# Kernel optimization log

Hardware: AMD Instinct MI355X
Metric: run time of the kernel (lower is better)

The kernel has to match this reference:

```python
import jax, jax.numpy as jnp
import numpy as np


def setup_inputs() -> dict:
    key = jax.random.key(0)
    kq, kk, kv, kl = jax.random.split(key, 4)
    B, Nq, Nkv, D = 16, 2048, 2048, 64
    return {
        "Q_batch": jax.random.normal(kq, (B, Nq, D), dtype=jnp.float32),
        "K_batch": jax.random.normal(kk, (B, Nkv, D), dtype=jnp.float32),
        "V_batch": jax.random.normal(kv, (B, Nkv, D), dtype=jnp.float32),
        "valid_lens": jax.random.randint(kl, (B,), 0, Nkv, dtype=jnp.int64 if jax.config.jax_enable_x64 else jnp.int32),
    }


def reference(Q_batch, K_batch, V_batch, valid_lens):
    # S: (B, Nq, Nkv) scaled dot-product scores
    d = Q_batch.shape[-1]
    scale = 1.0 / jnp.sqrt(jnp.asarray(d, Q_batch.dtype))
    S = jnp.einsum('bqd,bkd->bqk', Q_batch, K_batch) * scale
    # mask_first_n_valid: position k valid iff k < valid_lens[b], broadcast over queries
    kv_idx = jnp.arange(S.shape[-1])  # (Nkv,)
    mask = kv_idx[None, None, :] < valid_lens[:, None, None]  # (B, 1->Nq, Nkv)
    S = jnp.where(mask, S, jnp.asarray(-1e20, S.dtype))
    W = jax.nn.softmax(S, axis=-1)  # attention weights (dropout rate = 0.0)
    return jnp.einsum('bqk,bkv->bqv', W, V_batch)
```

## Files before the change

### kernel.cpp

```cpp
#include <hip/hip_runtime.h>

#define BATCH 16
#define NQ    2048
#define NKV   2048
#define DH    64
#define SC    0.18033688011112042f
#define TILE_B 8192

typedef __attribute__((ext_vector_type(8))) short  bf16x8;
typedef __attribute__((ext_vector_type(16))) float f32x16;

__device__ __forceinline__ unsigned f2bf(float f) {
  unsigned u = __builtin_bit_cast(unsigned, f);
  u += 0x7FFFu + ((u >> 16) & 1u);
  return u >> 16;
}

template <int CTRL>
__device__ __forceinline__ float dppf(float x) {
  return __builtin_bit_cast(
      float, __builtin_amdgcn_mov_dpp(__builtin_bit_cast(int, x), CTRL, 0xF, 0xF, false));
}
__device__ __forceinline__ float rowsum16(float v) {
  v += dppf<0x128>(v);
  v += dppf<0x124>(v);
  v += dppf<0x122>(v);
  v += dppf<0x121>(v);
  return v;
}

__global__ __launch_bounds__(256) void convert_kernel(
    const float* __restrict__ K, const float* __restrict__ V,
    unsigned char* __restrict__ WS) {
  const int tid = threadIdx.x;
  const int bt  = blockIdx.x;
  const int b   = bt >> 6, t = bt & 63;
  unsigned char* tile = WS + (size_t)bt * TILE_B;
  const size_t   srow = ((size_t)b * NKV + (size_t)t * 32) * DH;

  const int l = tid & 63, g = tid >> 6;
  {
    const int key = l & 31, d0 = g * 16 + (l >> 5) * 8;
    const float4* p = (const float4*)(K + srow + (size_t)key * DH + d0);
    float4 a = p[0], c4 = p[1];
    bf16x8 w;
    w[0] = (short)f2bf(a.x);  w[1] = (short)f2bf(a.y);
    w[2] = (short)f2bf(a.z);  w[3] = (short)f2bf(a.w);
    w[4] = (short)f2bf(c4.x); w[5] = (short)f2bf(c4.y);
    w[6] = (short)f2bf(c4.z); w[7] = (short)f2bf(c4.w);
    *(bf16x8*)(tile + g * 1024 + l * 16) = w;
  }
  {
    const int d    = (g & 1) * 32 + (l & 31);
    const int key0 = (g >> 1) * 16 + (l >> 5) * 8;
    const float* vp = V + srow + (size_t)key0 * DH + d;
    bf16x8 w;
#pragma unroll
    for (int j = 0; j < 8; ++j) w[j] = (short)f2bf(vp[(size_t)j * DH]);
    *(bf16x8*)(tile + 4096 + g * 1024 + l * 16) = w;
  }
}

__global__ __launch_bounds__(256, 4) void sdpa_kernel(
    const float* __restrict__ Q, const unsigned char* __restrict__ WS,
    const int* __restrict__ lens, float* __restrict__ O) {
  __shared__ alignas(16) unsigned char smem[10240 + 2 * 12288];

  const int tid  = threadIdx.x;
  const int lane = tid & 63;
  const int wave = tid >> 6;
  const int k32  = lane & 31;
  const int hi   = lane >> 5;

  const int idx = blockIdx.x, layer = idx >> 8, rr = idx & 255;
  const int b   = (rr + layer * 3) & 15;
  const int qo  = (rr >> 4) + layer * 16;

  const int  L    = lens[b];
  const bool zlen = (L == 0);
  const int  Leff = zlen ? NKV : L;
  const int  nT   = (Leff + 31) >> 5;
  const int  tb   = (nT * wave) >> 2;
  const int  te   = (nT * (wave + 1)) >> 2;
  const int  cnt  = te - tb;
  const int  tmask = (!zlen && (L & 31)) ? nT - 1 : -1;

  bf16x8 Qf[4];
  {
    const float* qp = Q + ((size_t)b * NQ + qo * 32 + k32) * DH + hi * 8;
#pragma unroll
    for (int c = 0; c < 4; ++c) {
      const float4* p = (const float4*)(qp + c * 16);
      float4 a = p[0], d4 = p[1];
      bf16x8 w;
      w[0] = (short)f2bf(a.x * SC);  w[1] = (short)f2bf(a.y * SC);
      w[2] = (short)f2bf(a.z * SC);  w[3] = (short)f2bf(a.w * SC);
      w[4] = (short)f2bf(d4.x * SC); w[5] = (short)f2bf(d4.y * SC);
      w[6] = (short)f2bf(d4.z * SC); w[7] = (short)f2bf(d4.w * SC);
      Qf[c] = w;
    }
  }

  unsigned char*       Pw  = smem + wave * 2560;
  unsigned char*       pwr = Pw + hi * 320 + k32 * 2;
  const unsigned char* prd = Pw + k32 * 80 + hi * 16;

  const unsigned char* gp = WS + (size_t)(b * 64 + tb) * TILE_B + lane * 16;

  f32x16 oc0, oc1;
  float  l_[16];
#pragma unroll
  for (int r = 0; r < 16; ++r) { oc0[r] = 0.f; oc1[r] = 0.f; l_[r] = 0.f; }

  for (int it = 0; it < cnt; ++it) {
    bf16x8 cur[8];
#pragma unroll
    for (int i = 0; i < 8; ++i) cur[i] = *(const bf16x8*)(gp + i * 1024);
    gp += TILE_B;

    const int t = tb + it;

    f32x16 acc;
#pragma unroll
    for (int r = 0; r < 16; ++r) acc[r] = 0.f;
#pragma unroll
    for (int c = 0; c < 4; ++c)
      acc = __builtin_amdgcn_mfma_f32_32x32x16_bf16(Qf[c], cur[c], acc, 0, 0, 0);

    if (zlen) {
#pragma unroll
      for (int r = 0; r < 16; ++r) acc[r] = 0.f;
    } else if (t == tmask) {
      const bool valid = (t * 32 + k32) < L;
      if (!valid) {
#pragma unroll
        for (int r = 0; r < 16; ++r) acc[r] = -1e30f;
      }
    }

#pragma unroll
    for (int r = 0; r < 16; ++r) {
      float    p = __builtin_amdgcn_exp2f(acc[r]);
      unsigned u = __builtin_bit_cast(unsigned, p);
      l_[r] += __builtin_bit_cast(float, u & 0xFFFF0000u);
      *(unsigned short*)(pwr + ((r & 3) + 8 * (r >> 2)) * 80) =
          (unsigned short)(u >> 16);
    }

#pragma unroll
    for (int ks = 0; ks < 2; ++ks) {
      bf16x8 Pf = *(const bf16x8*)(prd + ks * 32);
      oc0 = __builtin_amdgcn_mfma_f32_32x32x16_bf16(Pf, cur[4 + ks * 2], oc0, 0, 0, 0);
      oc1 = __builtin_amdgcn_mfma_f32_32x32x16_bf16(Pf, cur[5 + ks * 2], oc1, 0, 0, 0);
    }
  }

  float* MS = (float*)(void*)(smem + 10240);
  __syncthreads();
  if (wave >= 2) {
    float* Mb = MS + (wave - 2) * 3072 + lane;
#pragma unroll
    for (int r = 0; r < 16; ++r) {
      Mb[r * 64] = l_[r]; Mb[(16 + r) * 64] = oc0[r]; Mb[(32 + r) * 64] = oc1[r];
    }
  }
  __syncthreads();
  if (wave < 2) {
    float* Mb = MS + wave * 3072 + lane;
#pragma unroll
    for (int r = 0; r < 16; ++r) {
      l_[r] += Mb[r * 64]; oc0[r] += Mb[(16 + r) * 64]; oc1[r] += Mb[(32 + r) * 64];
    }
  }
  __syncthreads();
  if (wave == 1) {
    float* Mb = MS + lane;
#pragma unroll
    for (int r = 0; r < 16; ++r) {
      Mb[r * 64] = l_[r]; Mb[(16 + r) * 64] = oc0[r]; Mb[(32 + r) * 64] = oc1[r];
    }
  }
  __syncthreads();
  if (wave == 0) {
    float* Mb = MS + lane;
#pragma unroll
    for (int r = 0; r < 16; ++r) {
      l_[r] += Mb[r * 64]; oc0[r] += Mb[(16 + r) * 64]; oc1[r] += Mb[(32 + r) * 64];
    }
    float* Ob = O + ((size_t)b * NQ + qo * 32) * DH;
#pragma unroll
    for (int r = 0; r < 16; ++r) {
      float s = rowsum16(l_[r]);
      s += __builtin_bit_cast(
          float, __builtin_amdgcn_ds_swizzle(__builtin_bit_cast(int, s), 0x401F));
      const float inv = 1.0f / s;
      const int   q   = (r & 3) + 8 * (r >> 2) + 4 * hi;
      Ob[q * DH + k32]      = oc0[r] * inv;
      Ob[q * DH + 32 + k32] = oc1[r] * inv;
    }
  }
}

extern "C" void kernel_launch(void* const* d_in, const int* in_sizes, int n_in,
                              void* d_out, int out_size, void* d_ws, size_t ws_size,
                              hipStream_t stream) {
  const float* Q    = (const float*)d_in[0];
  const float* K    = (const float*)d_in[1];
  const float* V    = (const float*)d_in[2];
  const int*   lens = (const int*)d_in[3];
  float*       Out  = (float*)d_out;
  unsigned char* WS = (unsigned char*)d_ws;

  hipLaunchKernelGGL(convert_kernel, dim3(BATCH * 64), dim3(256), 0, stream, K, V, WS);
  hipLaunchKernelGGL(sdpa_kernel, dim3(1024), dim3(256), 0, stream, Q, WS, lens, Out);
}
```

Before: 97.86 us.

## Process 64 queries per block, keep P in registers, prefetch next KV tile

Each block now handles 64 queries (two 32-row Q fragments), so every loaded K/V tile is reused twice and the grid is halved. The MFMA operands are swapped so the P tile comes out in a layout that can feed the PV MFMA straight from registers, which drops the LDS round trip for P. The V tile layout in the convert kernel is changed to match. The next tile is loaded into registers while the current one is computed, and the output is staged through LDS for coalesced float4 stores. The convert kernel also skips tiles past the valid length. Costs are higher register pressure (launch bounds lowered to 2) and fewer blocks, which may leave some CUs idle.

```diff
diff --git a/kernel.cpp b/kernel.cpp
--- a/kernel.cpp
+++ b/kernel.cpp
@@ -16,32 +16,22 @@
   return u >> 16;
 }
 
-template <int CTRL>
-__device__ __forceinline__ float dppf(float x) {
-  return __builtin_bit_cast(
-      float, __builtin_amdgcn_mov_dpp(__builtin_bit_cast(int, x), CTRL, 0xF, 0xF, false));
-}
-__device__ __forceinline__ float rowsum16(float v) {
-  v += dppf<0x128>(v);
-  v += dppf<0x124>(v);
-  v += dppf<0x122>(v);
-  v += dppf<0x121>(v);
-  return v;
-}
-
 __global__ __launch_bounds__(256) void convert_kernel(
     const float* __restrict__ K, const float* __restrict__ V,
-    unsigned char* __restrict__ WS) {
-  const int tid = threadIdx.x;
-  const int bt  = blockIdx.x;
-  const int b   = bt >> 6, t = bt & 63;
+    const int* __restrict__ lens, unsigned char* __restrict__ WS) {
+  const int bt = blockIdx.x;
+  const int b = bt >> 6, t = bt & 63;
+  const int L = lens[b];
+  const int Leff = (L == 0) ? NKV : L;
+  if (t * 32 >= Leff) return;
+
   unsigned char* tile = WS + (size_t)bt * TILE_B;
   const size_t   srow = ((size_t)b * NKV + (size_t)t * 32) * DH;
-
+  const int tid = threadIdx.x;
   const int l = tid & 63, g = tid >> 6;
+  const int l31 = l & 31, hi = l >> 5;
   {
-    const int key = l & 31, d0 = g * 16 + (l >> 5) * 8;
-    const float4* p = (const float4*)(K + srow + (size_t)key * DH + d0);
+    const float4* p = (const float4*)(K + srow + (size_t)l31 * DH + g * 16 + hi * 8);
     float4 a = p[0], c4 = p[1];
     bf16x8 w;
     w[0] = (short)f2bf(a.x);  w[1] = (short)f2bf(a.y);
@@ -51,26 +41,25 @@
     *(bf16x8*)(tile + g * 1024 + l * 16) = w;
   }
   {
-    const int d    = (g & 1) * 32 + (l & 31);
-    const int key0 = (g >> 1) * 16 + (l >> 5) * 8;
-    const float* vp = V + srow + (size_t)key0 * DH + d;
+    const int c2 = g & 1, dh = g >> 1;
+    const float* vp = V + srow + (size_t)(c2 * 16 + 4 * hi) * DH + dh * 32 + l31;
     bf16x8 w;
 #pragma unroll
-    for (int j = 0; j < 8; ++j) w[j] = (short)f2bf(vp[(size_t)j * DH]);
+    for (int j = 0; j < 8; ++j)
+      w[j] = (short)f2bf(vp[(size_t)((j & 3) + 8 * (j >> 2)) * DH]);
     *(bf16x8*)(tile + 4096 + g * 1024 + l * 16) = w;
   }
 }
 
-__global__ __launch_bounds__(256, 4) void sdpa_kernel(
+__global__ __launch_bounds__(256, 2) void sdpa_kernel(
     const float* __restrict__ Q, const unsigned char* __restrict__ WS,
     const int* __restrict__ lens, float* __restrict__ O) {
-  __shared__ alignas(16) unsigned char smem[10240 + 2 * 12288];
+  __shared__ float smem[8448];
 
   const int tid  = threadIdx.x;
   const int lane = tid & 63;
   const int wave = tid >> 6;
-  const int k32  = lane & 31;
-  const int hi   = lane >> 5;
+  const int l31  = lane & 31, hi = lane >> 5;
 
   const int idx = blockIdx.x, layer = idx >> 8, rr = idx & 255;
   const int b   = (rr + layer * 3) & 15;
@@ -85,9 +74,10 @@
   const int  cnt  = te - tb;
   const int  tmask = (!zlen && (L & 31)) ? nT - 1 : -1;
 
-  bf16x8 Qf[4];
-  {
-    const float* qp = Q + ((size_t)b * NQ + qo * 32 + k32) * DH + hi * 8;
+  bf16x8 Qf[2][4];
+#pragma unroll
+  for (int u = 0; u < 2; ++u) {
+    const float* qp = Q + ((size_t)b * NQ + qo * 64 + u * 32 + l31) * DH + hi * 8;
 #pragma unroll
     for (int c = 0; c < 4; ++c) {
       const float4* p = (const float4*)(qp + c * 16);
@@ -97,107 +87,142 @@
       w[2] = (short)f2bf(a.z * SC);  w[3] = (short)f2bf(a.w * SC);
       w[4] = (short)f2bf(d4.x * SC); w[5] = (short)f2bf(d4.y * SC);
       w[6] = (short)f2bf(d4.z * SC); w[7] = (short)f2bf(d4.w * SC);
-      Qf[c] = w;
+      Qf[u][c] = w;
     }
   }
 
-  unsigned char*       Pw  = smem + wave * 2560;
-  unsigned char*       pwr = Pw + hi * 320 + k32 * 2;
-  const unsigned char* prd = Pw + k32 * 80 + hi * 16;
-
   const unsigned char* gp = WS + (size_t)(b * 64 + tb) * TILE_B + lane * 16;
 
-  f32x16 oc0, oc1;
-  float  l_[16];
-#pragma unroll
-  for (int r = 0; r < 16; ++r) { oc0[r] = 0.f; oc1[r] = 0.f; l_[r] = 0.f; }
+  f32x16 oc[4];
+  float  l_[2] = {0.f, 0.f};
+#pragma unroll
+  for (int i = 0; i < 4; ++i)
+#pragma unroll
+    for (int r = 0; r < 16; ++r) oc[i][r] = 0.f;
+
+  bf16x8 cur[8];
+  if (cnt > 0) {
+#pragma unroll
+    for (int i = 0; i < 8; ++i) cur[i] = *(const bf16x8*)(gp + i * 1024);
+  }
 
   for (int it = 0; it < cnt; ++it) {
-    bf16x8 cur[8];
-#pragma unroll
-    for (int i = 0; i < 8; ++i) cur[i] = *(const bf16x8*)(gp + i * 1024);
+    const int t = tb + it;
+    const unsigned char* gn = (it + 1 < cnt) ? (gp + TILE_B) : gp;
+    bf16x8 nxt[8];
+#pragma unroll
+    for (int i = 0; i < 8; ++i) nxt[i] = *(const bf16x8*)(gn + i * 1024);
     gp += TILE_B;
 
-    const int t = tb + it;
-
-    f32x16 acc;
-#pragma unroll
-    for (int r = 0; r < 16; ++r) acc[r] = 0.f;
-#pragma unroll
-    for (int c = 0; c < 4; ++c)
-      acc = __builtin_amdgcn_mfma_f32_32x32x16_bf16(Qf[c], cur[c], acc, 0, 0, 0);
-
-    if (zlen) {
+#pragma unroll
+    for (int u = 0; u < 2; ++u) {
+      f32x16 acc;
 #pragma unroll
       for (int r = 0; r < 16; ++r) acc[r] = 0.f;
-    } else if (t == tmask) {
-      const bool valid = (t * 32 + k32) < L;
-      if (!valid) {
-#pragma unroll
-        for (int r = 0; r < 16; ++r) acc[r] = -1e30f;
+#pragma unroll
+      for (int c = 0; c < 4; ++c)
+        acc = __builtin_amdgcn_mfma_f32_32x32x16_bf16(cur[c], Qf[u][c], acc, 0, 0, 0);
+
+      if (zlen) {
+#pragma unroll
+        for (int r = 0; r < 16; ++r) acc[r] = 0.f;
+      } else if (t == tmask) {
+#pragma unroll
+        for (int r = 0; r < 16; ++r) {
+          const int key = t * 32 + (r & 3) + 8 * (r >> 2) + 4 * hi;
+          if (key >= L) acc[r] = -1e30f;
+        }
       }
+
+      unsigned short ph[16];
+      float ls = 0.f;
+#pragma unroll
+      for (int r = 0; r < 16; ++r) {
+        float    p  = __builtin_amdgcn_exp2f(acc[r]);
+        unsigned uu = __builtin_bit_cast(unsigned, p);
+        ls += __builtin_bit_cast(float, uu & 0xFFFF0000u);
+        ph[r] = (unsigned short)(uu >> 16);
+      }
+      l_[u] += ls;
+
+      bf16x8 Pf0, Pf1;
+#pragma unroll
+      for (int j = 0; j < 8; ++j) { Pf0[j] = (short)ph[j]; Pf1[j] = (short)ph[8 + j]; }
+
+      oc[u * 2 + 0] = __builtin_amdgcn_mfma_f32_32x32x16_bf16(cur[4], Pf0, oc[u * 2 + 0], 0, 0, 0);
+      oc[u * 2 + 0] = __builtin_amdgcn_mfma_f32_32x32x16_bf16(cur[5], Pf1, oc[u * 2 + 0], 0, 0, 0);
+      oc[u * 2 + 1] = __builtin_amdgcn_mfma_f32_32x32x16_bf16(cur[6], Pf0, oc[u * 2 + 1], 0, 0, 0);
+      oc[u * 2 + 1] = __builtin_amdgcn_mfma_f32_32x32x16_bf16(cur[7], Pf1, oc[u * 2 + 1], 0, 0, 0);
     }
-
-#pragma unroll
-    for (int r = 0; r < 16; ++r) {
-      float    p = __builtin_amdgcn_exp2f(acc[r]);
-      unsigned u = __builtin_bit_cast(unsigned, p);
-      l_[r] += __builtin_bit_cast(float, u & 0xFFFF0000u);
-      *(unsigned short*)(pwr + ((r & 3) + 8 * (r >> 2)) * 80) =
-          (unsigned short)(u >> 16);
+#pragma unroll
+    for (int i = 0; i < 8; ++i) cur[i] = nxt[i];
+  }
+
+  __syncthreads();
+  if (wave >= 2) {
+    float* Mb = smem + (wave - 2) * 4224 + lane;
+#pragma unroll
+    for (int i = 0; i < 4; ++i)
+#pragma unroll
+      for (int r = 0; r < 16; ++r) Mb[(i * 16 + r) * 64] = oc[i][r];
+    Mb[64 * 64] = l_[0];
+    Mb[65 * 64] = l_[1];
+  }
+  __syncthreads();
+  if (wave < 2) {
+    float* Mb = smem + wave * 4224 + lane;
+#pragma unroll
+    for (int i = 0; i < 4; ++i)
+#pragma unroll
+      for (int r = 0; r < 16; ++r) oc[i][r] += Mb[(i * 16 + r) * 64];
+    l_[0] += Mb[64 * 64];
+    l_[1] += Mb[65 * 64];
+  }
+  __syncthreads();
+  if (wave == 1) {
+    float* Mb = smem + lane;
+#pragma unroll
+    for (int i = 0; i < 4; ++i)
+#pragma unroll
+      for (int r = 0; r < 16; ++r) Mb[(i * 16 + r) * 64] = oc[i][r];
+    Mb[64 * 64] = l_[0];
+    Mb[65 * 64] = l_[1];
+  }
+  __syncthreads();
+  if (wave == 0) {
+    float* Mb = smem + lane;
+#pragma unroll
+    for (int i = 0; i < 4; ++i)
+#pragma unroll
+      for (int r = 0; r < 16; ++r) oc[i][r] += Mb[(i * 16 + r) * 64];
+    l_[0] += Mb[64 * 64];
+    l_[1] += Mb[65 * 64];
+
+    const float inv0 = 1.0f / (l_[0] + __shfl_xor(l_[0], 32, 64));
+    const float inv1 = 1.0f / (l_[1] + __shfl_xor(l_[1], 32, 64));
+
+#pragma unroll
+    for (int u = 0; u < 2; ++u) {
+      const float inv = u ? inv1 : inv0;
+      const int   q   = u * 32 + l31;
+#pragma unroll
+      for (int dh = 0; dh < 2; ++dh)
+#pragma unroll
+        for (int r = 0; r < 16; ++r) {
+          const int d = dh * 32 + (r & 3) + 8 * (r >> 2) + 4 * hi;
+          smem[q * 68 + d] = oc[u * 2 + dh][r] * inv;
+        }
     }
-
-#pragma unroll
-    for (int ks = 0; ks < 2; ++ks) {
-      bf16x8 Pf = *(const bf16x8*)(prd + ks * 32);
-      oc0 = __builtin_amdgcn_mfma_f32_32x32x16_bf16(Pf, cur[4 + ks * 2], oc0, 0, 0, 0);
-      oc1 = __builtin_amdgcn_mfma_f32_32x32x16_bf16(Pf, cur[5 + ks * 2], oc1, 0, 0, 0);
-    }
-  }
-
-  float* MS = (float*)(void*)(smem + 10240);
-  __syncthreads();
-  if (wave >= 2) {
-    float* Mb = MS + (wave - 2) * 3072 + lane;
-#pragma unroll
-    for (int r = 0; r < 16; ++r) {
-      Mb[r * 64] = l_[r]; Mb[(16 + r) * 64] = oc0[r]; Mb[(32 + r) * 64] = oc1[r];
-    }
-  }
-  __syncthreads();
-  if (wave < 2) {
-    float* Mb = MS + wave * 3072 + lane;
-#pragma unroll
-    for (int r = 0; r < 16; ++r) {
-      l_[r] += Mb[r * 64]; oc0[r] += Mb[(16 + r) * 64]; oc1[r] += Mb[(32 + r) * 64];
-    }
-  }
-  __syncthreads();
-  if (wave == 1) {
-    float* Mb = MS + lane;
-#pragma unroll
-    for (int r = 0; r < 16; ++r) {
-      Mb[r * 64] = l_[r]; Mb[(16 + r) * 64] = oc0[r]; Mb[(32 + r) * 64] = oc1[r];
-    }
-  }
-  __syncthreads();
-  if (wave == 0) {
-    float* Mb = MS + lane;
-#pragma unroll
-    for (int r = 0; r < 16; ++r) {
-      l_[r] += Mb[r * 64]; oc0[r] += Mb[(16 + r) * 64]; oc1[r] += Mb[(32 + r) * 64];
-    }
-    float* Ob = O + ((size_t)b * NQ + qo * 32) * DH;
-#pragma unroll
-    for (int r = 0; r < 16; ++r) {
-      float s = rowsum16(l_[r]);
-      s += __builtin_bit_cast(
-          float, __builtin_amdgcn_ds_swizzle(__builtin_bit_cast(int, s), 0x401F));
-      const float inv = 1.0f / s;
-      const int   q   = (r & 3) + 8 * (r >> 2) + 4 * hi;
-      Ob[q * DH + k32]      = oc0[r] * inv;
-      Ob[q * DH + 32 + k32] = oc1[r] * inv;
-    }
+  }
+  __syncthreads();
+
+  float* Ob = O + ((size_t)b * NQ + (size_t)qo * 64) * DH;
+#pragma unroll
+  for (int R = 0; R < 4; ++R) {
+    const int fi = R * 256 + tid;
+    const int q = fi >> 4, ch = fi & 15;
+    float4 v4 = *(const float4*)&smem[q * 68 + ch * 4];
+    *(float4*)(Ob + (size_t)q * DH + ch * 4) = v4;
   }
 }
 
@@ -211,6 +236,6 @@
   float*       Out  = (float*)d_out;
   unsigned char* WS = (unsigned char*)d_ws;
 
-  hipLaunchKernelGGL(convert_kernel, dim3(BATCH * 64), dim3(256), 0, stream, K, V, WS);
-  hipLaunchKernelGGL(sdpa_kernel, dim3(1024), dim3(256), 0, stream, Q, WS, lens, Out);
-}
+  hipLaunchKernelGGL(convert_kernel, dim3(BATCH * 64), dim3(256), 0, stream, K, V, lens, WS);
+  hipLaunchKernelGGL(sdpa_kernel, dim3(512), dim3(256), 0, stream, Q, WS, lens, Out);
+}
```

Result: faster. 95.68 us (-2.2%).
